# Kernel tuning notes

Measured on AMD Instinct MI355X. Metric: run time of the kernel, lower is better.

The kernel has to match this reference:

```python
import jax, jax.numpy as jnp
import numpy as np
import math

B, L, D, A, VD, H = 8, 2048, 1024, 1024, 1024, 1024
EPS = 1e-5

def gelu(x):
    return 0.5 * x * (1.0 + jax.lax.erf(x / math.sqrt(2.0)))

def setup_inputs() -> dict:
    key = jax.random.key(0)
    ks = jax.random.split(key, 12)
    s = 0.02
    return {
        "Q": jax.random.normal(ks[0], (B, L, D), jnp.float32),
        "K": jax.random.normal(ks[1], (B, L, D), jnp.float32),
        "V": jax.random.normal(ks[2], (B, L, D), jnp.float32),
        "attn_mask": jax.random.randint(ks[3], (B, L, L), 0, 2, jnp.int32),
        "Wq": jax.random.normal(ks[4], (D, A), jnp.float32) * s,
        "bq": jnp.zeros((A,), jnp.float32),
        "Wk": jax.random.normal(ks[5], (D, A), jnp.float32) * s,
        "bk": jnp.zeros((A,), jnp.float32),
        "Wv": jax.random.normal(ks[6], (D, VD), jnp.float32) * s,
        "bv": jnp.zeros((VD,), jnp.float32),
        "Wo": jax.random.normal(ks[7], (VD, H), jnp.float32) * s,
        "bo": jnp.zeros((H,), jnp.float32),
        "gamma": jnp.ones((H,), jnp.float32),
        "beta": jnp.zeros((H,), jnp.float32),
    }

def reference(Q, K, V, attn_mask, Wq, bq, Wk, bk, Wv, bv, Wo, bo, gamma, beta):
    q = Q @ Wq + bq                      # [B,L,A]
    k = K @ Wk + bk                      # [B,L,A]
    scores = jnp.einsum('bqa,bka->bqk', q, k) / math.sqrt(A)
    scores = scores + attn_mask.astype(jnp.float32) * (-1e9)
    scores = jnp.swapaxes(scores, -1, -2)  # [B,Lk,Lq]; softmax over QUERY axis
    attn = jax.nn.softmax(scores, axis=-1)
    wv = V @ Wv + bv                     # [B,L,VD]
    context = jnp.einsum('bkq,bqv->bkv', attn, wv)  # [B,L,VD]
    context = gelu(context @ Wo + bo)    # [B,L,H]
    mu = jnp.mean(context, axis=-1, keepdims=True)
    var = jnp.var(context, axis=-1, keepdims=True)
    context = (context - mu) / jnp.sqrt(var + EPS) * gamma + beta
    return context, attn
```

## Files before the change

### kernel.cpp

```cpp
#include <hip/hip_runtime.h>
#include <math.h>

typedef __bf16 bf16;
typedef __bf16 bf16x8 __attribute__((ext_vector_type(8)));
typedef __bf16 bf16x4 __attribute__((ext_vector_type(4)));
typedef float f32x4 __attribute__((ext_vector_type(4)));

__device__ inline void gload16(const void* g, void* l) {
  typedef __attribute__((address_space(1))) const unsigned int guint;
  typedef __attribute__((address_space(3))) unsigned int luint;
  __builtin_amdgcn_global_load_lds((guint*)g, (luint*)l, 16, 0, 0);
}

template<int BIAS_MODE, bool MASK, bool GELU, bool OUT_BF16>
__global__ __launch_bounds__(512, 2)
void bgemm8_k(const bf16* __restrict__ A, const bf16* __restrict__ B,
              const float* __restrict__ bias, const signed char* __restrict__ mT,
              void* __restrict__ Cout, int N, int K,
              long sAb, long sBb, long sCb, long sMb, float scale)
{
  __shared__ bf16 As[4 * 8192];
  __shared__ bf16 Bs[4 * 8192];

  const int t    = threadIdx.x;
  const int zb   = blockIdx.z;
  const int gx   = gridDim.x;
  const int nwg  = gx * gridDim.y;
  const int orig = blockIdx.y * gx + blockIdx.x;
  const int swz  = (orig & 7) * (nwg >> 3) + (orig >> 3);
  const int m0   = (swz / gx) * 256;
  const int n0   = (swz % gx) * 256;

  const int wave = t >> 6;
  const int lane = t & 63;
  const int wm = wave >> 2;
  const int wn = wave & 3;
  const int fr = lane & 15;
  const int fg = lane >> 4;

  const bf16* Abase = A + (size_t)zb * sAb + (size_t)m0 * K;
  const bf16* Bbase = B + (size_t)zb * sBb + (size_t)n0 * K;
  size_t gOff[2];
  int    ldsOff[2];
#pragma unroll
  for (int j = 0; j < 2; ++j) {
    const int L   = j * 8192 + t * 16;
    const int row = L >> 6;
    const int gp  = (L >> 4) & 3;
    const int g   = gp ^ ((row >> 1) & 3);
    gOff[j]   = (size_t)row * K + (size_t)g * 8;
    ldsOff[j] = j * 4096 + wave * 512;
  }
  const int HMAX = (K >> 5) * 2;

  auto stage = [&](int H) {
    if (H >= HMAX) return;
    const int s    = H >> 1;
    const int slot = s & 3;
    const size_t kof = (size_t)s * 32;
    if ((H & 1) == 0) {
      gload16(Abase + kof + gOff[0], As + slot * 8192 + ldsOff[0]);
      gload16(Abase + kof + gOff[1], As + slot * 8192 + ldsOff[1]);
    } else {
      gload16(Bbase + kof + gOff[0], Bs + slot * 8192 + ldsOff[0]);
      gload16(Bbase + kof + gOff[1], Bs + slot * 8192 + ldsOff[1]);
    }
  };

  const int xsw  = (fg ^ ((fr >> 1) & 3)) * 8;
  const int aoff = (wm * 128 + fr) * 32 + xsw;
  const int boff = (wn * 64 + fr) * 32 + xsw;

  f32x4 acc[8][4] = {};
  const int T = K >> 6;

  stage(0); stage(1); stage(2); stage(3); stage(4);
  asm volatile("s_waitcnt vmcnt(2)" ::: "memory");
  asm volatile("s_barrier" ::: "memory");

  for (int tt = 0; tt < T; ++tt) {
#pragma unroll
    for (int p = 0; p < 4; ++p) {
      const int kk   = p & 1;
      const int oh   = p >> 1;
      const int slot = (2 * tt + kk) & 3;
      bf16x8 af[4], bfv[4];
#pragma unroll
      for (int i = 0; i < 4; ++i)
        af[i]  = *(const bf16x8*)(As + slot * 8192 + aoff + (oh * 4 + i) * 512);
#pragma unroll
      for (int i = 0; i < 4; ++i)
        bfv[i] = *(const bf16x8*)(Bs + slot * 8192 + boff + i * 512);
      stage(4 * tt + p + 5);
      asm volatile("s_barrier" ::: "memory");
      __builtin_amdgcn_s_setprio(1);
#pragma unroll
      for (int mi = 0; mi < 4; ++mi)
#pragma unroll
        for (int ni = 0; ni < 4; ++ni)
          acc[oh * 4 + mi][ni] =
            __builtin_amdgcn_mfma_f32_16x16x32_bf16(af[mi], bfv[ni], acc[oh * 4 + mi][ni], 0, 0, 0);
      __builtin_amdgcn_s_setprio(0);
      if (p == 3) {
        if (tt >= T - 2) asm volatile("s_waitcnt vmcnt(0)" ::: "memory");
        else             asm volatile("s_waitcnt vmcnt(2)" ::: "memory");
      }
      asm volatile("s_barrier" ::: "memory");
    }
  }

  const signed char* mb = mT + (size_t)zb * sMb;
#pragma unroll
  for (int mi = 0; mi < 8; ++mi) {
#pragma unroll
    for (int ni = 0; ni < 4; ++ni) {
      const int col = n0 + wn * 64 + ni * 16 + fr;
#pragma unroll
      for (int i = 0; i < 4; ++i) {
        const int r = m0 + wm * 128 + mi * 16 + fg * 4 + i;
        float v = acc[mi][ni][i] * scale;
        if constexpr (BIAS_MODE == 1) v += bias[col];
        if constexpr (BIAS_MODE == 2) v += bias[r];
        if constexpr (MASK) v += -1e9f * (float)mb[(size_t)r * N + col];
        if constexpr (GELU) v = 0.5f * v * (1.0f + erff(v * 0.70710678118f));
        const size_t off = (size_t)zb * sCb + (size_t)r * N + col;
        if constexpr (OUT_BF16) ((bf16*)Cout)[off] = (bf16)v;
        else                    ((float*)Cout)[off] = v;
      }
    }
  }
}

__global__ __launch_bounds__(256)
void conv_k(const float* __restrict__ in, bf16* __restrict__ out, long n8)
{
  for (long i = blockIdx.x * 256 + threadIdx.x; i < n8; i += (long)gridDim.x * 256) {
    f32x4 a = *(const f32x4*)(in + i * 8);
    f32x4 b = *(const f32x4*)(in + i * 8 + 4);
    bf16x8 o;
#pragma unroll
    for (int j = 0; j < 4; ++j) { o[j] = (bf16)a[j]; o[4 + j] = (bf16)b[j]; }
    *(bf16x8*)(out + i * 8) = o;
  }
}

__global__ __launch_bounds__(256)
void wtrans_k(const float* __restrict__ W0, const float* __restrict__ W1,
              const float* __restrict__ W2, const float* __restrict__ W3,
              bf16* __restrict__ out)
{
  const float* Ws[4] = {W0, W1, W2, W3};
  const float* W = Ws[blockIdx.z];
  bf16* o = out + (size_t)blockIdx.z * (1024 * 1024);
  __shared__ bf16 tile[64][72];
  const int t  = threadIdx.x;
  const int c0 = blockIdx.x * 64;
  const int r0 = blockIdx.y * 64;
  {
    const int rr = t >> 2;
    const int cc = (t & 3) * 16;
    const float* src = W + (size_t)(r0 + rr) * 1024 + c0 + cc;
#pragma unroll
    for (int j = 0; j < 16; j += 4) {
      f32x4 v = *(const f32x4*)(src + j);
#pragma unroll
      for (int i = 0; i < 4; ++i) tile[cc + j + i][rr] = (bf16)v[i];
    }
  }
  __syncthreads();
  {
    const int nr = t >> 2;
    const int kc = (t & 3) * 16;
    bf16* dst = o + (size_t)(c0 + nr) * 1024 + r0 + kc;
    *(bf16x8*)dst       = *(const bf16x8*)&tile[nr][kc];
    *(bf16x8*)(dst + 8) = *(const bf16x8*)&tile[nr][kc + 8];
  }
}

__global__ __launch_bounds__(256)
void maskT_k(const int* __restrict__ mask, signed char* __restrict__ mT)
{
  __shared__ signed char tile[64][65];
  const int t  = threadIdx.x;
  const int b  = blockIdx.z;
  const int k0 = blockIdx.x * 64;
  const int q0 = blockIdx.y * 64;
  {
    const int iq = t >> 2;
    const int ic = (t & 3) * 16;
    const int* src = mask + ((size_t)b * 2048 + q0 + iq) * 2048 + k0 + ic;
#pragma unroll
    for (int j = 0; j < 16; j += 4) {
      int4 v = *(const int4*)(src + j);
      tile[ic + j + 0][iq] = (signed char)v.x;
      tile[ic + j + 1][iq] = (signed char)v.y;
      tile[ic + j + 2][iq] = (signed char)v.z;
      tile[ic + j + 3][iq] = (signed char)v.w;
    }
  }
  __syncthreads();
  {
    const int ik = t >> 2;
    const int iq = (t & 3) * 16;
    signed char* dst = mT + ((size_t)b * 2048 + k0 + ik) * 2048 + q0 + iq;
#pragma unroll
    for (int j = 0; j < 16; ++j) dst[j] = tile[ik][iq + j];
  }
}

__global__ __launch_bounds__(256)
void softmax_rows_k(float* __restrict__ P, bf16* __restrict__ Pb)
{
  float* p = P + (size_t)blockIdx.x * 2048;
  bf16*  pb = Pb + (size_t)blockIdx.x * 2048;
  const int t = threadIdx.x;
  const int wave = t >> 6, lane = t & 63;
  f32x4 v0 = *(const f32x4*)(p + t * 4);
  f32x4 v1 = *(const f32x4*)(p + 1024 + t * 4);
  float m = -3e38f;
#pragma unroll
  for (int j = 0; j < 4; ++j) { m = fmaxf(m, v0[j]); m = fmaxf(m, v1[j]); }
#pragma unroll
  for (int off = 32; off; off >>= 1) m = fmaxf(m, __shfl_xor(m, off));
  __shared__ float red[8];
  if (lane == 0) red[wave] = m;
  __syncthreads();
  m = fmaxf(fmaxf(red[0], red[1]), fmaxf(red[2], red[3]));
  float s = 0.0f;
#pragma unroll
  for (int j = 0; j < 4; ++j) {
    v0[j] = __expf(v0[j] - m); s += v0[j];
    v1[j] = __expf(v1[j] - m); s += v1[j];
  }
#pragma unroll
  for (int off = 32; off; off >>= 1) s += __shfl_xor(s, off);
  if (lane == 0) red[4 + wave] = s;
  __syncthreads();
  s = red[4] + red[5] + red[6] + red[7];
  const float inv = 1.0f / s;
  bf16x4 b0, b1;
#pragma unroll
  for (int j = 0; j < 4; ++j) {
    v0[j] *= inv; v1[j] *= inv;
    b0[j] = (bf16)v0[j]; b1[j] = (bf16)v1[j];
  }
  *(f32x4*)(p + t * 4)        = v0;
  *(f32x4*)(p + 1024 + t * 4) = v1;
  *(bf16x4*)(pb + t * 4)        = b0;
  *(bf16x4*)(pb + 1024 + t * 4) = b1;
}

__global__ __launch_bounds__(256)
void ln_k(const float* __restrict__ g, const float* __restrict__ gamma,
          const float* __restrict__ beta, float* __restrict__ out)
{
  const float* p = g + (size_t)blockIdx.x * 1024;
  const int t = threadIdx.x;
  const int wave = t >> 6, lane = t & 63;
  f32x4 v = *(const f32x4*)(p + t * 4);
  float s = v[0] + v[1] + v[2] + v[3];
  float q = v[0]*v[0] + v[1]*v[1] + v[2]*v[2] + v[3]*v[3];
#pragma unroll
  for (int off = 32; off; off >>= 1) { s += __shfl_xor(s, off); q += __shfl_xor(q, off); }
  __shared__ float red[16];
  if (lane == 0) { red[wave] = s; red[8 + wave] = q; }
  __syncthreads();
  s = red[0] + red[1] + red[2] + red[3];
  q = red[8] + red[9] + red[10] + red[11];
  const float mu   = s * (1.0f / 1024.0f);
  const float var  = q * (1.0f / 1024.0f) - mu * mu;
  const float rstd = rsqrtf(var + 1e-5f);
  f32x4 gm = *(const f32x4*)(gamma + t * 4);
  f32x4 bt = *(const f32x4*)(beta + t * 4);
  f32x4 o;
#pragma unroll
  for (int j = 0; j < 4; ++j) o[j] = (v[j] - mu) * rstd * gm[j] + bt[j];
  *(f32x4*)(out + (size_t)blockIdx.x * 1024 + t * 4) = o;
}

extern "C" void kernel_launch(void* const* d_in, const int* in_sizes, int n_in,
                              void* d_out, int out_size, void* d_ws, size_t ws_size,
                              hipStream_t stream)
{
  const float* Q     = (const float*)d_in[0];
  const float* Kin   = (const float*)d_in[1];
  const float* V     = (const float*)d_in[2];
  const int*   mask  = (const int*)d_in[3];
  const float* Wq    = (const float*)d_in[4];
  const float* bq    = (const float*)d_in[5];
  const float* Wk    = (const float*)d_in[6];
  const float* bk    = (const float*)d_in[7];
  const float* Wv    = (const float*)d_in[8];
  const float* bv    = (const float*)d_in[9];
  const float* Wo    = (const float*)d_in[10];
  const float* bo    = (const float*)d_in[11];
  const float* gamma = (const float*)d_in[12];
  const float* beta  = (const float*)d_in[13];

  float* outCtx  = (float*)d_out;
  float* outAttn = outCtx + (size_t)8 * 2048 * 1024;

  char* ws = (char*)d_ws;
  const size_t MB = 1048576;
  bf16*        wts   = (bf16*)(ws + 0 * MB);
  bf16*        qp    = (bf16*)(ws + 8 * MB);
  bf16*        kp    = (bf16*)(ws + 40 * MB);
  bf16*        Qb    = (bf16*)(ws + 72 * MB);
  bf16*        Kb    = (bf16*)(ws + 104 * MB);
  signed char* mT    = (signed char*)(ws + 72 * MB);
  bf16*        attnb = (bf16*)(ws + 40 * MB);
  bf16*        wvT   = (bf16*)(ws + 8 * MB);
  bf16*        Vb    = (bf16*)(ws + 104 * MB);
  bf16*        ctx   = (bf16*)(ws + 104 * MB);
  float*       g     = (float*)(ws + 40 * MB);
  bf16* Wqt = wts;
  bf16* Wkt = wts + 1 * 1024 * 1024;
  bf16* Wvt = wts + 2 * 1024 * 1024;
  bf16* Wot = wts + 3 * 1024 * 1024;

  const dim3 blk(256);
  const dim3 blk8(512);
  const long n8 = (long)16384 * 1024 / 8;

  wtrans_k<<<dim3(16, 16, 4), blk, 0, stream>>>(Wq, Wk, Wv, Wo, wts);
  conv_k<<<dim3(2048), blk, 0, stream>>>(Q, Qb, n8);
  conv_k<<<dim3(2048), blk, 0, stream>>>(Kin, Kb, n8);
  bgemm8_k<1, false, false, true><<<dim3(4, 64, 1), blk8, 0, stream>>>(
      Qb, Wqt, bq, nullptr, qp, 1024, 1024, 0, 0, 0, 0, 1.0f);
  bgemm8_k<1, false, false, true><<<dim3(4, 64, 1), blk8, 0, stream>>>(
      Kb, Wkt, bk, nullptr, kp, 1024, 1024, 0, 0, 0, 0, 1.0f);
  conv_k<<<dim3(2048), blk, 0, stream>>>(V, Vb, n8);
  maskT_k<<<dim3(32, 32, 8), blk, 0, stream>>>(mask, mT);
  bgemm8_k<0, true, false, false><<<dim3(8, 8, 8), blk8, 0, stream>>>(
      kp, qp, nullptr, mT, outAttn, 2048, 1024,
      (long)2048 * 1024, (long)2048 * 1024, (long)2048 * 2048, (long)2048 * 2048, 0.03125f);
  bgemm8_k<2, false, false, true><<<dim3(8, 4, 8), blk8, 0, stream>>>(
      Wvt, Vb, bv, nullptr, wvT, 2048, 1024,
      0, (long)2048 * 1024, (long)1024 * 2048, 0, 1.0f);
  softmax_rows_k<<<dim3(16384), blk, 0, stream>>>(outAttn, attnb);
  bgemm8_k<0, false, false, true><<<dim3(4, 8, 8), blk8, 0, stream>>>(
      attnb, wvT, nullptr, nullptr, ctx, 1024, 2048,
      (long)2048 * 2048, (long)1024 * 2048, (long)2048 * 1024, 0, 1.0f);
  bgemm8_k<1, false, true, false><<<dim3(4, 64, 1), blk8, 0, stream>>>(
      ctx, Wot, bo, nullptr, g, 1024, 1024, 0, 0, 0, 0, 1.0f);
  ln_k<<<dim3(16384), blk, 0, stream>>>(g, gamma, beta, outCtx);
}
```

Baseline: 534.2 us.

## Store attention scores and GELU output as bf16 and deepen GEMM load pipelining

```diff
diff --git a/kernel.cpp b/kernel.cpp
--- a/kernel.cpp
+++ b/kernel.cpp
@@ -16,7 +16,7 @@
 __global__ __launch_bounds__(512, 2)
 void bgemm8_k(const bf16* __restrict__ A, const bf16* __restrict__ B,
               const float* __restrict__ bias, const signed char* __restrict__ mT,
-              void* __restrict__ Cout, int N, int K,
+              void* __restrict__ Cout, int N, int ldc, int K,
               long sAb, long sBb, long sCb, long sMb, float scale)
 {
   __shared__ bf16 As[4 * 8192];
@@ -75,8 +75,8 @@
   const int T = K >> 6;
 
   stage(0); stage(1); stage(2); stage(3); stage(4);
-  asm volatile("s_waitcnt vmcnt(2)" ::: "memory");
-  asm volatile("s_barrier" ::: "memory");
+  asm volatile("s_waitcnt vmcnt(6)" ::: "memory");
+  __builtin_amdgcn_s_barrier();
 
   for (int tt = 0; tt < T; ++tt) {
 #pragma unroll
@@ -92,7 +92,7 @@
       for (int i = 0; i < 4; ++i)
         bfv[i] = *(const bf16x8*)(Bs + slot * 8192 + boff + i * 512);
       stage(4 * tt + p + 5);
-      asm volatile("s_barrier" ::: "memory");
+      __builtin_amdgcn_s_barrier();
       __builtin_amdgcn_s_setprio(1);
 #pragma unroll
       for (int mi = 0; mi < 4; ++mi)
@@ -101,11 +101,15 @@
           acc[oh * 4 + mi][ni] =
             __builtin_amdgcn_mfma_f32_16x16x32_bf16(af[mi], bfv[ni], acc[oh * 4 + mi][ni], 0, 0, 0);
       __builtin_amdgcn_s_setprio(0);
+      if (p == 0) {
+        if (tt == T - 1) asm volatile("s_waitcnt vmcnt(0)" ::: "memory");
+        else             asm volatile("s_waitcnt vmcnt(4)" ::: "memory");
+      }
       if (p == 3) {
-        if (tt >= T - 2) asm volatile("s_waitcnt vmcnt(0)" ::: "memory");
-        else             asm volatile("s_waitcnt vmcnt(2)" ::: "memory");
+        if (tt < T - 2)       asm volatile("s_waitcnt vmcnt(6)" ::: "memory");
+        else if (tt == T - 2) asm volatile("s_waitcnt vmcnt(4)" ::: "memory");
       }
-      asm volatile("s_barrier" ::: "memory");
+      __builtin_amdgcn_s_barrier();
     }
   }
 
@@ -123,7 +127,7 @@
         if constexpr (BIAS_MODE == 2) v += bias[r];
         if constexpr (MASK) v += -1e9f * (float)mb[(size_t)r * N + col];
         if constexpr (GELU) v = 0.5f * v * (1.0f + erff(v * 0.70710678118f));
-        const size_t off = (size_t)zb * sCb + (size_t)r * N + col;
+        const size_t off = (size_t)zb * sCb + (size_t)r * ldc + col;
         if constexpr (OUT_BF16) ((bf16*)Cout)[off] = (bf16)v;
         else                    ((float*)Cout)[off] = v;
       }
@@ -211,15 +215,19 @@
 __global__ __launch_bounds__(256)
 void softmax_rows_k(float* __restrict__ P, bf16* __restrict__ Pb)
 {
-  float* p = P + (size_t)blockIdx.x * 2048;
-  bf16*  pb = Pb + (size_t)blockIdx.x * 2048;
+  char* slot = (char*)P + (size_t)blockIdx.x * 8192;
+  const bf16* pin = (const bf16*)slot;
+  float* pout = (float*)slot;
+  bf16* pb = Pb + (size_t)blockIdx.x * 2048;
   const int t = threadIdx.x;
   const int wave = t >> 6, lane = t & 63;
-  f32x4 v0 = *(const f32x4*)(p + t * 4);
-  f32x4 v1 = *(const f32x4*)(p + 1024 + t * 4);
+  bf16x8 raw = *(const bf16x8*)(pin + t * 8);
+  float v[8];
+#pragma unroll
+  for (int j = 0; j < 8; ++j) v[j] = (float)raw[j];
   float m = -3e38f;
 #pragma unroll
-  for (int j = 0; j < 4; ++j) { m = fmaxf(m, v0[j]); m = fmaxf(m, v1[j]); }
+  for (int j = 0; j < 8; ++j) m = fmaxf(m, v[j]);
 #pragma unroll
   for (int off = 32; off; off >>= 1) m = fmaxf(m, __shfl_xor(m, off));
   __shared__ float red[8];
@@ -228,36 +236,37 @@
   m = fmaxf(fmaxf(red[0], red[1]), fmaxf(red[2], red[3]));
   float s = 0.0f;
 #pragma unroll
-  for (int j = 0; j < 4; ++j) {
-    v0[j] = __expf(v0[j] - m); s += v0[j];
-    v1[j] = __expf(v1[j] - m); s += v1[j];
-  }
+  for (int j = 0; j < 8; ++j) { v[j] = __expf(v[j] - m); s += v[j]; }
 #pragma unroll
   for (int off = 32; off; off >>= 1) s += __shfl_xor(s, off);
   if (lane == 0) red[4 + wave] = s;
   __syncthreads();
   s = red[4] + red[5] + red[6] + red[7];
   const float inv = 1.0f / s;
-  bf16x4 b0, b1;
+  f32x4 o0, o1;
+  bf16x8 ob;
 #pragma unroll
   for (int j = 0; j < 4; ++j) {
-    v0[j] *= inv; v1[j] *= inv;
-    b0[j] = (bf16)v0[j]; b1[j] = (bf16)v1[j];
-  }
-  *(f32x4*)(p + t * 4)        = v0;
-  *(f32x4*)(p + 1024 + t * 4) = v1;
-  *(bf16x4*)(pb + t * 4)        = b0;
-  *(bf16x4*)(pb + 1024 + t * 4) = b1;
-}
-
-__global__ __launch_bounds__(256)
-void ln_k(const float* __restrict__ g, const float* __restrict__ gamma,
+    o0[j] = v[j] * inv; o1[j] = v[4 + j] * inv;
+    ob[j] = (bf16)o0[j]; ob[4 + j] = (bf16)o1[j];
+  }
+  __syncthreads();
+  *(f32x4*)(pout + t * 8)     = o0;
+  *(f32x4*)(pout + t * 8 + 4) = o1;
+  *(bf16x8*)(pb + t * 8)      = ob;
+}
+
+__global__ __launch_bounds__(256)
+void ln_k(const bf16* __restrict__ g, const float* __restrict__ gamma,
           const float* __restrict__ beta, float* __restrict__ out)
 {
-  const float* p = g + (size_t)blockIdx.x * 1024;
+  const bf16* p = g + (size_t)blockIdx.x * 1024;
   const int t = threadIdx.x;
   const int wave = t >> 6, lane = t & 63;
-  f32x4 v = *(const f32x4*)(p + t * 4);
+  bf16x4 raw = *(const bf16x4*)(p + t * 4);
+  f32x4 v;
+#pragma unroll
+  for (int j = 0; j < 4; ++j) v[j] = (float)raw[j];
   float s = v[0] + v[1] + v[2] + v[3];
   float q = v[0]*v[0] + v[1]*v[1] + v[2]*v[2] + v[3]*v[3];
 #pragma unroll
@@ -312,7 +321,7 @@
   bf16*        wvT   = (bf16*)(ws + 8 * MB);
   bf16*        Vb    = (bf16*)(ws + 104 * MB);
   bf16*        ctx   = (bf16*)(ws + 104 * MB);
-  float*       g     = (float*)(ws + 40 * MB);
+  bf16*        g     = (bf16*)(ws + 40 * MB);
   bf16* Wqt = wts;
   bf16* Wkt = wts + 1 * 1024 * 1024;
   bf16* Wvt = wts + 2 * 1024 * 1024;
@@ -326,22 +335,22 @@
   conv_k<<<dim3(2048), blk, 0, stream>>>(Q, Qb, n8);
   conv_k<<<dim3(2048), blk, 0, stream>>>(Kin, Kb, n8);
   bgemm8_k<1, false, false, true><<<dim3(4, 64, 1), blk8, 0, stream>>>(
-      Qb, Wqt, bq, nullptr, qp, 1024, 1024, 0, 0, 0, 0, 1.0f);
+      Qb, Wqt, bq, nullptr, qp, 1024, 1024, 1024, 0, 0, 0, 0, 1.0f);
   bgemm8_k<1, false, false, true><<<dim3(4, 64, 1), blk8, 0, stream>>>(
-      Kb, Wkt, bk, nullptr, kp, 1024, 1024, 0, 0, 0, 0, 1.0f);
+      Kb, Wkt, bk, nullptr, kp, 1024, 1024, 1024, 0, 0, 0, 0, 1.0f);
   conv_k<<<dim3(2048), blk, 0, stream>>>(V, Vb, n8);
   maskT_k<<<dim3(32, 32, 8), blk, 0, stream>>>(mask, mT);
-  bgemm8_k<0, true, false, false><<<dim3(8, 8, 8), blk8, 0, stream>>>(
-      kp, qp, nullptr, mT, outAttn, 2048, 1024,
-      (long)2048 * 1024, (long)2048 * 1024, (long)2048 * 2048, (long)2048 * 2048, 0.03125f);
+  bgemm8_k<0, true, false, true><<<dim3(8, 8, 8), blk8, 0, stream>>>(
+      kp, qp, nullptr, mT, (bf16*)outAttn, 2048, 4096, 1024,
+      (long)2048 * 1024, (long)2048 * 1024, (long)2048 * 4096, (long)2048 * 2048, 0.03125f);
   bgemm8_k<2, false, false, true><<<dim3(8, 4, 8), blk8, 0, stream>>>(
-      Wvt, Vb, bv, nullptr, wvT, 2048, 1024,
+      Wvt, Vb, bv, nullptr, wvT, 2048, 2048, 1024,
       0, (long)2048 * 1024, (long)1024 * 2048, 0, 1.0f);
   softmax_rows_k<<<dim3(16384), blk, 0, stream>>>(outAttn, attnb);
   bgemm8_k<0, false, false, true><<<dim3(4, 8, 8), blk8, 0, stream>>>(
-      attnb, wvT, nullptr, nullptr, ctx, 1024, 2048,
+      attnb, wvT, nullptr, nullptr, ctx, 1024, 1024, 2048,
       (long)2048 * 2048, (long)1024 * 2048, (long)2048 * 1024, 0, 1.0f);
-  bgemm8_k<1, false, true, false><<<dim3(4, 64, 1), blk8, 0, stream>>>(
-      ctx, Wot, bo, nullptr, g, 1024, 1024, 0, 0, 0, 0, 1.0f);
+  bgemm8_k<1, false, true, true><<<dim3(4, 64, 1), blk8, 0, stream>>>(
+      ctx, Wot, bo, nullptr, g, 1024, 1024, 1024, 0, 0, 0, 0, 1.0f);
   ln_k<<<dim3(16384), blk, 0, stream>>>(g, gamma, beta, outCtx);
 }
```

Result: faster. 505.9 us (-5.3%).
